# Kernel tuning notes

Measured on AMD Instinct MI355X. Metric: run time of the kernel, lower is better.

Reference implementation:

```python
import jax, jax.numpy as jnp
import numpy as np

N, E, G = 50000, 1000000, 8
H, C, L = 4, 32, 3          # heads, per-head channels, GAT layers
HID = H * C                  # 128
NODE_D, EDGE_D, REC_D = 64, 16, 8
NEG_SLOPE = 0.2              # PyG GATConv default


def setup_inputs() -> dict:
    key = jax.random.key(0)
    ks = jax.random.split(key, 24)

    def glorot(k, shape):
        fan_in = shape[-2] if len(shape) >= 2 else shape[-1]
        return jax.random.normal(k, shape, dtype=jnp.float32) / jnp.sqrt(jnp.float32(fan_in))

    inp = {
        "x": jax.random.normal(ks[0], (N, NODE_D), dtype=jnp.float32),
        "edge_index": jax.random.randint(ks[1], (2, E), 0, N, dtype=jnp.int64),
        "edge_attr": jax.random.normal(ks[2], (E, EDGE_D), dtype=jnp.float32),
        "batch": jnp.sort(jax.random.randint(ks[3], (N,), 0, G, dtype=jnp.int64)),
        "recipe": jax.random.normal(ks[4], (G, REC_D), dtype=jnp.float32),
        # input projection + edge encoder
        "W_in": glorot(ks[5], (NODE_D + REC_D, HID)),
        "b_in": jnp.zeros((HID,), jnp.float32),
        "W_edge": glorot(ks[6], (EDGE_D, HID)),
        "b_edge": jnp.zeros((HID,), jnp.float32),
        # stacked GATConv params (PyG GATConv: lin & lin_edge have no bias)
        "lin_w": glorot(ks[7], (L, HID, HID)),
        "lin_edge_w": glorot(ks[8], (L, HID, HID)),
        "att_src": glorot(ks[9], (L, H, C)),
        "att_dst": glorot(ks[10], (L, H, C)),
        "att_edge": glorot(ks[11], (L, H, C)),
        "gat_bias": jnp.zeros((L, HID), jnp.float32),
        "W1": glorot(ks[12], (HID, HID)),
        "b1": jnp.zeros((HID,), jnp.float32),
        "W2": glorot(ks[13], (HID, 1)),
        "b2": jnp.zeros((1,), jnp.float32),
    }
    return inp


def reference(x, edge_index, edge_attr, batch, recipe,
              W_in, b_in, W_edge, b_edge,
              lin_w, lin_edge_w, att_src, att_dst, att_edge, gat_bias,
              W1, b1, W2, b2):
    src, dst = edge_index[0], edge_index[1]

    # broadcast recipe to nodes, project, relu
    h = jnp.concatenate([x, recipe[batch]], axis=1)        # [N, NODE_D+REC_D]
    h = jax.nn.relu(h @ W_in + b_in)                        # [N, HID]
    e = edge_attr @ W_edge + b_edge                         # [E, HID]

    for l in range(L):
        xl = (h @ lin_w[l]).reshape(N, H, C)                # [N,H,C]
        el = (e @ lin_edge_w[l]).reshape(E, H, C)           # [E,H,C]
        a_src = jnp.sum(xl * att_src[l], axis=-1)           # [N,H]
        a_dst = jnp.sum(xl * att_dst[l], axis=-1)           # [N,H]
        a_edge = jnp.sum(el * att_edge[l], axis=-1)         # [E,H]
        alpha = jax.nn.leaky_relu(a_src[src] + a_dst[dst] + a_edge, NEG_SLOPE)
        # segment softmax over destination nodes
        amax = jax.ops.segment_max(alpha, dst, num_segments=N)   # [N,H]
        alpha = jnp.exp(alpha - amax[dst])
        denom = jax.ops.segment_sum(alpha, dst, num_segments=N)  # [N,H]
        alpha = alpha / denom[dst]
        # weighted message scatter-add (dropout is identity in eval mode)
        msg = xl[src] * alpha[..., None]                    # [E,H,C]
        out = jax.ops.segment_sum(msg, dst, num_segments=N).reshape(N, HID) + gat_bias[l]
        h = jax.nn.relu(out)

    # global mean pool over graphs
    counts = jax.ops.segment_sum(jnp.ones((N,), h.dtype), batch, num_segments=G)
    g = jax.ops.segment_sum(h, batch, num_segments=G) / jnp.maximum(counts, 1.0)[:, None]

    return jax.nn.relu(g @ W1 + b1) @ W2 + b2               # [G,1]
```

## Files before the change

kernel.cpp:

```cpp
#include <hip/hip_runtime.h>
#include <math.h>


__device__ __forceinline__ float lrelu(float x) { return x >= 0.f ? x : 0.2f * x; }

__device__ __forceinline__ unsigned pack_bf2(float a, float b) {
  unsigned ua = __float_as_uint(a), ub = __float_as_uint(b);
  ua += 0x7fffu + ((ua >> 16) & 1u);
  ub += 0x7fffu + ((ub >> 16) & 1u);
  return (ua >> 16) | (ub & 0xffff0000u);
}
__device__ __forceinline__ float bf_lo(unsigned u) { return __uint_as_float(u << 16); }
__device__ __forceinline__ float bf_hi(unsigned u) { return __uint_as_float(u & 0xffff0000u); }

__global__ void rank_kernel(const int* __restrict__ dst, int* __restrict__ deg,
                            int* __restrict__ rank, int E) {
  int e = blockIdx.x * 256 + threadIdx.x;
  if (e < E) rank[e] = atomicAdd(&deg[dst[e]], 1);
}

__global__ __launch_bounds__(1024) void scanA_kernel(const int* __restrict__ deg,
                                                     int* __restrict__ tmp,
                                                     int* __restrict__ bsum, int n) {
  __shared__ int wsum[16];
  int tid = threadIdx.x;
  int lane = tid & 63, wid = tid >> 6;
  int i = blockIdx.x * 1024 + tid;
  int v = (i < n) ? deg[i] : 0;
  int sv = v;
#pragma unroll
  for (int off = 1; off < 64; off <<= 1) {
    int t = __shfl_up(sv, off);
    if (lane >= off) sv += t;
  }
  if (lane == 63) wsum[wid] = sv;
  __syncthreads();
  if (wid == 0) {
    int wv = (lane < 16) ? wsum[lane] : 0;
#pragma unroll
    for (int off = 1; off < 16; off <<= 1) {
      int t = __shfl_up(wv, off);
      if (lane >= off) wv += t;
    }
    if (lane < 16) wsum[lane] = wv;
  }
  __syncthreads();
  int waveoff = (wid > 0) ? wsum[wid - 1] : 0;
  int incl = waveoff + sv;
  if (i < n) tmp[i] = incl;
  if (tid == 1023) bsum[blockIdx.x] = incl;
}

__global__ void scanB_kernel(int* __restrict__ bsum, int nb, int* __restrict__ total_out) {
  int lane = threadIdx.x;
  int v = (lane < nb) ? bsum[lane] : 0;
  int sv = v;
#pragma unroll
  for (int off = 1; off < 64; off <<= 1) {
    int t = __shfl_up(sv, off);
    if (lane >= off) sv += t;
  }
  if (lane < nb) bsum[lane] = sv - v;
  if (lane == 63) *total_out = sv;
}

__global__ __launch_bounds__(1024) void scanC_kernel(const int* __restrict__ deg,
                                                     const int* __restrict__ tmp,
                                                     const int* __restrict__ bsum,
                                                     int* __restrict__ row_ptr, int n) {
  int i = blockIdx.x * 1024 + threadIdx.x;
  if (i < n) row_ptr[i] = tmp[i] - deg[i] + bsum[blockIdx.x];
}

__global__ void perm_kernel(const int* __restrict__ dst, const int* __restrict__ rank,
                            const int* __restrict__ row_ptr, int* __restrict__ perm, int E) {
  int e = blockIdx.x * 256 + threadIdx.x;
  if (e < E) perm[row_ptr[dst[e]] + rank[e]] = e;
}

__global__ void prep_params(const float* __restrict__ lin_edge_w,
                            const float* __restrict__ att_edge,
                            const float* __restrict__ W_edge,
                            const float* __restrict__ b_edge,
                            float* __restrict__ Mc) {
  __shared__ float WE[128][12];
  int t = threadIdx.x;
  for (int idx = t; idx < 128 * 12; idx += 256) {
    int k = idx / 12, j = idx - k * 12;
    int l = j >> 2, h = j & 3;
    float s = 0.f;
    for (int c = 0; c < 32; ++c)
      s += lin_edge_w[((size_t)l * 128 + k) * 128 + h * 32 + c] * att_edge[(l * 4 + h) * 32 + c];
    WE[k][j] = s;
  }
  __syncthreads();
  for (int idx = t; idx < 16 * 12; idx += 256) {
    int i = idx / 12, j = idx - i * 12;
    float s = 0.f;
    for (int k = 0; k < 128; ++k) s += W_edge[i * 128 + k] * WE[k][j];
    Mc[idx] = s;
  }
  if (t < 12) {
    float s = 0.f;
    for (int k = 0; k < 128; ++k) s += b_edge[k] * WE[k][t];
    Mc[192 + t] = s;
  }
}

__global__ void edge_build_kernel(const int* __restrict__ perm,
                                  const int* __restrict__ srcA,
                                  const float* __restrict__ edge_attr,
                                  const float* __restrict__ Mc,
                                  int* __restrict__ src_csr,
                                  float* __restrict__ a_edge_csr, int E) {
  __shared__ float M[16][12];
  __shared__ float cv[12];
  int t = threadIdx.x;
  if (t < 192) M[t / 12][t % 12] = Mc[t];
  if (t < 12) cv[t] = Mc[192 + t];
  __syncthreads();
  int i = blockIdx.x * 256 + t;
  if (i >= E) return;
  int e = perm[i];
  const float4* p = (const float4*)(edge_attr + (size_t)e * 16);
  float4 v0 = p[0], v1 = p[1], v2 = p[2], v3 = p[3];
  float ea[16] = {v0.x, v0.y, v0.z, v0.w, v1.x, v1.y, v1.z, v1.w,
                  v2.x, v2.y, v2.z, v2.w, v3.x, v3.y, v3.z, v3.w};
  float a[12];
#pragma unroll
  for (int j = 0; j < 12; ++j) {
    float s = cv[j];
#pragma unroll
    for (int k = 0; k < 16; ++k) s += ea[k] * M[k][j];
    a[j] = s;
  }
  src_csr[i] = srcA[e];
#pragma unroll
  for (int l = 0; l < 3; ++l) {
    float4 o = make_float4(a[l * 4 + 0], a[l * 4 + 1], a[l * 4 + 2], a[l * 4 + 3]);
    *(float4*)(a_edge_csr + ((size_t)l * E + i) * 4) = o;
  }
}

__global__ __launch_bounds__(256) void proj_kernel(const float* __restrict__ x,
                                                   const float* __restrict__ recipe,
                                                   const int* __restrict__ batch,
                                                   const float* __restrict__ W_in,
                                                   const float* __restrict__ b_in,
                                                   float* __restrict__ h, int N) {
  __shared__ float Wc[72][128];
  __shared__ float Ac[64][72];
  int t = threadIdx.x;
  int tx = t & 31, ty = t >> 5;
  int row0 = blockIdx.x * 64;
  for (int idx = t; idx < 2304; idx += 256) {
    int k = idx >> 5, c4 = idx & 31;
    *(float4*)&Wc[k][c4 * 4] = *(const float4*)(W_in + (size_t)k * 128 + c4 * 4);
  }
  for (int idx = t; idx < 1024; idx += 256) {
    int r = idx >> 4, c4 = idx & 15;
    int row = row0 + r;
    float4 v = make_float4(0.f, 0.f, 0.f, 0.f);
    if (row < N) v = *(const float4*)(x + (size_t)row * 64 + c4 * 4);
    *(float4*)&Ac[r][c4 * 4] = v;
  }
  for (int idx = t; idx < 128; idx += 256) {
    int r = idx >> 1, c4 = idx & 1;
    int row = row0 + r;
    float4 v = make_float4(0.f, 0.f, 0.f, 0.f);
    if (row < N) v = *(const float4*)(recipe + (size_t)batch[row] * 8 + c4 * 4);
    *(float4*)&Ac[r][64 + c4 * 4] = v;
  }
  __syncthreads();
  float4 bias = *(const float4*)(b_in + tx * 4);
  float4 acc[8];
#pragma unroll
  for (int s = 0; s < 8; ++s) acc[s] = bias;
  for (int k4 = 0; k4 < 18; ++k4) {
    float4 w0 = *(float4*)&Wc[k4 * 4 + 0][tx * 4];
    float4 w1 = *(float4*)&Wc[k4 * 4 + 1][tx * 4];
    float4 w2 = *(float4*)&Wc[k4 * 4 + 2][tx * 4];
    float4 w3 = *(float4*)&Wc[k4 * 4 + 3][tx * 4];
#pragma unroll
    for (int s = 0; s < 8; ++s) {
      float4 av = *(float4*)&Ac[ty + 8 * s][k4 * 4];
      acc[s].x += av.x * w0.x + av.y * w1.x + av.z * w2.x + av.w * w3.x;
      acc[s].y += av.x * w0.y + av.y * w1.y + av.z * w2.y + av.w * w3.y;
      acc[s].z += av.x * w0.z + av.y * w1.z + av.z * w2.z + av.w * w3.z;
      acc[s].w += av.x * w0.w + av.y * w1.w + av.z * w2.w + av.w * w3.w;
    }
  }
#pragma unroll
  for (int s = 0; s < 8; ++s) {
    int row = row0 + ty + 8 * s;
    if (row < N) {
      float4 o = acc[s];
      o.x = fmaxf(o.x, 0.f); o.y = fmaxf(o.y, 0.f);
      o.z = fmaxf(o.z, 0.f); o.w = fmaxf(o.w, 0.f);
      *(float4*)(h + (size_t)row * 128 + tx * 4) = o;
    }
  }
}

__global__ __launch_bounds__(256) void gemm128_kernel(const float* __restrict__ A,
                                                      const float* __restrict__ W,
                                                      const float* __restrict__ att_s,
                                                      const float* __restrict__ att_d,
                                                      unsigned short* __restrict__ Cb,
                                                      float* __restrict__ a_src,
                                                      float* __restrict__ a_dst, int M) {
  __shared__ float Wc[32][128];
  __shared__ float Ac[64][32];
  int t = threadIdx.x;
  int tx = t & 31, ty = t >> 5;
  int row0 = blockIdx.x * 64;
  float4 acc[8];
#pragma unroll
  for (int s = 0; s < 8; ++s) acc[s] = make_float4(0.f, 0.f, 0.f, 0.f);
  for (int kc = 0; kc < 128; kc += 32) {
    for (int idx = t; idx < 1024; idx += 256) {
      int k = idx >> 5, c4 = idx & 31;
      *(float4*)&Wc[k][c4 * 4] = *(const float4*)(W + (size_t)(kc + k) * 128 + c4 * 4);
    }
    for (int idx = t; idx < 512; idx += 256) {
      int r = idx >> 3, c4 = idx & 7;
      int row = row0 + r;
      float4 v = make_float4(0.f, 0.f, 0.f, 0.f);
      if (row < M) v = *(const float4*)(A + (size_t)row * 128 + kc + c4 * 4);
      *(float4*)&Ac[r][c4 * 4] = v;
    }
    __syncthreads();
#pragma unroll
    for (int k4 = 0; k4 < 8; ++k4) {
      float4 w0 = *(float4*)&Wc[k4 * 4 + 0][tx * 4];
      float4 w1 = *(float4*)&Wc[k4 * 4 + 1][tx * 4];
      float4 w2 = *(float4*)&Wc[k4 * 4 + 2][tx * 4];
      float4 w3 = *(float4*)&Wc[k4 * 4 + 3][tx * 4];
#pragma unroll
      for (int s = 0; s < 8; ++s) {
        float4 av = *(float4*)&Ac[ty + 8 * s][k4 * 4];
        acc[s].x += av.x * w0.x + av.y * w1.x + av.z * w2.x + av.w * w3.x;
        acc[s].y += av.x * w0.y + av.y * w1.y + av.z * w2.y + av.w * w3.y;
        acc[s].z += av.x * w0.z + av.y * w1.z + av.z * w2.z + av.w * w3.z;
        acc[s].w += av.x * w0.w + av.y * w1.w + av.z * w2.w + av.w * w3.w;
      }
    }
    __syncthreads();
  }
  int hh = tx >> 3, sub = tx & 7;
  const float4 as4 = *(const float4*)(att_s + hh * 32 + sub * 4);
  const float4 ad4 = *(const float4*)(att_d + hh * 32 + sub * 4);
  float* part_s = &Wc[0][0];
  float* part_d = &Wc[16][0];
#pragma unroll
  for (int s = 0; s < 8; ++s) {
    int r = ty + 8 * s;
    int row = row0 + r;
    if (row < M) {
      uint2 pk;
      pk.x = pack_bf2(acc[s].x, acc[s].y);
      pk.y = pack_bf2(acc[s].z, acc[s].w);
      *(uint2*)(Cb + (size_t)row * 128 + tx * 4) = pk;
    }
    part_s[(r * 4 + hh) * 8 + sub] =
        acc[s].x * as4.x + acc[s].y * as4.y + acc[s].z * as4.z + acc[s].w * as4.w;
    part_d[(r * 4 + hh) * 8 + sub] =
        acc[s].x * ad4.x + acc[s].y * ad4.y + acc[s].z * ad4.z + acc[s].w * ad4.w;
  }
  __syncthreads();
  {
    int r = t >> 2, hd = t & 3;
    float ss = 0.f, dd = 0.f;
#pragma unroll
    for (int u = 0; u < 8; ++u) {
      ss += part_s[(r * 4 + hd) * 8 + u];
      dd += part_d[(r * 4 + hd) * 8 + u];
    }
    int row = row0 + r;
    if (row < M) {
      a_src[(size_t)row * 4 + hd] = ss;
      a_dst[(size_t)row * 4 + hd] = dd;
    }
  }
}

__global__ __launch_bounds__(256) void node_kernel(const int* __restrict__ row_ptr,
                                                   const int* __restrict__ src_csr,
                                                   const float* __restrict__ a_src,
                                                   const float* __restrict__ a_dst,
                                                   const float* __restrict__ aep,
                                                   const unsigned short* __restrict__ xlb,
                                                   const float* __restrict__ bias,
                                                   float* __restrict__ h_out, int N) {
  int lane = threadIdx.x & 63;
  int g = lane >> 3;
  int t = lane & 7;
  int h = t >> 1;
  int n = blockIdx.x * 4 + (threadIdx.x >> 6);
  if (n >= N) return;
  int s = row_ptr[n], e = row_ptr[n + 1];

  const float* bp = bias + t * 16;
  float* op = h_out + (size_t)n * 128 + t * 16;
  if (e <= s) {
    if (g == 0) {
#pragma unroll
      for (int q = 0; q < 4; ++q) {
        float4 b = *(const float4*)(bp + q * 4);
        float4 o = make_float4(fmaxf(b.x, 0.f), fmaxf(b.y, 0.f), fmaxf(b.z, 0.f), fmaxf(b.w, 0.f));
        *(float4*)(op + q * 4) = o;
      }
    }
    return;
  }

  float ad = a_dst[(size_t)n * 4 + h];

  float den = 0.f;
  float num[16];
#pragma unroll
  for (int c = 0; c < 16; ++c) num[c] = 0.f;

  for (int i = s + g; i < e; i += 8) {
    int sc = src_csr[i];
    float as = a_src[(size_t)sc * 4 + h];
    float ae = aep[(size_t)i * 4 + h];
    const uint4* xp = (const uint4*)(xlb + (size_t)sc * 128 + t * 16);
    uint4 u0 = xp[0], u1 = xp[1];
    float a = lrelu(as + ad + ae);
    float w = __expf(fminf(a, 80.f));
    den += w;
    num[0]  += w * bf_lo(u0.x); num[1]  += w * bf_hi(u0.x);
    num[2]  += w * bf_lo(u0.y); num[3]  += w * bf_hi(u0.y);
    num[4]  += w * bf_lo(u0.z); num[5]  += w * bf_hi(u0.z);
    num[6]  += w * bf_lo(u0.w); num[7]  += w * bf_hi(u0.w);
    num[8]  += w * bf_lo(u1.x); num[9]  += w * bf_hi(u1.x);
    num[10] += w * bf_lo(u1.y); num[11] += w * bf_hi(u1.y);
    num[12] += w * bf_lo(u1.z); num[13] += w * bf_hi(u1.z);
    num[14] += w * bf_lo(u1.w); num[15] += w * bf_hi(u1.w);
  }

#pragma unroll
  for (int off = 8; off < 64; off <<= 1) {
    den += __shfl_xor(den, off);
#pragma unroll
    for (int c = 0; c < 16; ++c) num[c] += __shfl_xor(num[c], off);
  }

  if (g == 0) {
    float rh = 1.f / den;
#pragma unroll
    for (int q = 0; q < 4; ++q) {
      float4 b = *(const float4*)(bp + q * 4);
      float4 o;
      o.x = fmaxf(num[q * 4 + 0] * rh + b.x, 0.f);
      o.y = fmaxf(num[q * 4 + 1] * rh + b.y, 0.f);
      o.z = fmaxf(num[q * 4 + 2] * rh + b.z, 0.f);
      o.w = fmaxf(num[q * 4 + 3] * rh + b.w, 0.f);
      *(float4*)(op + q * 4) = o;
    }
  }
}

__global__ void pool_kernel(const float* __restrict__ h, const int* __restrict__ batch,
                            float* __restrict__ g_sum, int* __restrict__ counts, int N) {
  int ch = threadIdx.x & 127;
  int sub = threadIdx.x >> 7;
  int per_block = (N + gridDim.x - 1) / gridDim.x;
  int start = blockIdx.x * per_block;
  int end = start + per_block;
  if (end > N) end = N;
  float acc = 0.f;
  int cnt = 0;
  int cur_g = -1;
  for (int i = start + sub; i < end; i += 2) {
    int g = batch[i];
    if (g != cur_g) {
      if (cur_g >= 0) {
        atomicAdd(&g_sum[(size_t)cur_g * 128 + ch], acc);
        if (ch == 0) atomicAdd(&counts[cur_g], cnt);
      }
      acc = 0.f;
      cnt = 0;
      cur_g = g;
    }
    acc += h[(size_t)i * 128 + ch];
    cnt += 1;
  }
  if (cur_g >= 0) {
    atomicAdd(&g_sum[(size_t)cur_g * 128 + ch], acc);
    if (ch == 0) atomicAdd(&counts[cur_g], cnt);
  }
}

__global__ void head_kernel(const float* __restrict__ g_sum, const int* __restrict__ counts,
                            const float* __restrict__ W1, const float* __restrict__ b1,
                            const float* __restrict__ W2, const float* __restrict__ b2,
                            float* __restrict__ out) {
  __shared__ float g[8][128];
  __shared__ float t1[8][128];
  int t = threadIdx.x;
  for (int idx = t; idx < 1024; idx += 256) {
    int gi = idx >> 7, ch = idx & 127;
    g[gi][ch] = g_sum[idx] / fmaxf((float)counts[gi], 1.f);
  }
  __syncthreads();
  for (int idx = t; idx < 1024; idx += 256) {
    int gi = idx >> 7, j = idx & 127;
    float a = b1[j];
    for (int k = 0; k < 128; ++k) a += g[gi][k] * W1[(size_t)k * 128 + j];
    t1[gi][j] = fmaxf(a, 0.f);
  }
  __syncthreads();
  if (t < 8) {
    float a = b2[0];
    for (int j = 0; j < 128; ++j) a += t1[t][j] * W2[j];
    out[t] = a;
  }
}

extern "C" void kernel_launch(void* const* d_in, const int* in_sizes, int n_in,
                              void* d_out, int out_size, void* d_ws, size_t ws_size,
                              hipStream_t stream) {
  const float* x         = (const float*)d_in[0];
  const int*   edge_idx  = (const int*)d_in[1];
  const float* edge_attr = (const float*)d_in[2];
  const int*   batch     = (const int*)d_in[3];
  const float* recipe    = (const float*)d_in[4];
  const float* W_in      = (const float*)d_in[5];
  const float* b_in      = (const float*)d_in[6];
  const float* W_edge    = (const float*)d_in[7];
  const float* b_edge    = (const float*)d_in[8];
  const float* lin_w     = (const float*)d_in[9];
  const float* lin_edge_w= (const float*)d_in[10];
  const float* att_src   = (const float*)d_in[11];
  const float* att_dst   = (const float*)d_in[12];
  const float* att_edge  = (const float*)d_in[13];
  const float* gat_bias  = (const float*)d_in[14];
  const float* W1        = (const float*)d_in[15];
  const float* b1        = (const float*)d_in[16];
  const float* W2        = (const float*)d_in[17];
  const float* b2p       = (const float*)d_in[18];

  const int N = in_sizes[3];
  const int E = in_sizes[1] / 2;
  const int* src = edge_idx;
  const int* dst = edge_idx + E;

  char* ws = (char*)d_ws;
  size_t off = 0;
  auto alloc = [&](size_t bytes) -> void* {
    void* p = ws + off;
    off += (bytes + 255) & ~(size_t)255;
    return p;
  };
  float* hA         = (float*)alloc((size_t)N * 128 * 4);
  float* hB         = (float*)alloc((size_t)N * 128 * 4);
  unsigned short* xlb = (unsigned short*)alloc((size_t)N * 128 * 2);
  float* a_srcA     = (float*)alloc((size_t)N * 4 * 4);
  float* a_dstA     = (float*)alloc((size_t)N * 4 * 4);
  float* a_edge_csr = (float*)alloc((size_t)3 * E * 4 * 4);
  int*   src_csr    = (int*)alloc((size_t)E * 4);
  int*   rank       = (int*)alloc((size_t)E * 4);
  int*   perm       = (int*)alloc((size_t)E * 4);
  int*   row_ptr    = (int*)alloc((size_t)(N + 1) * 4);
  int*   deg        = (int*)alloc((size_t)N * 4);
  int*   scan_tmp   = (int*)alloc((size_t)N * 4);
  int*   bsum       = (int*)alloc(64 * 4);
  float* Mc         = (float*)alloc(204 * 4);
  float* g_sum      = (float*)alloc(8 * 128 * 4);
  int*   counts     = (int*)alloc(8 * 4);
  (void)ws_size; (void)n_in; (void)out_size;

  const int eb = (E + 255) / 256;
  const int rowtiles = (N + 63) / 64;
  const int nb = (N + 1023) / 1024;

  hipMemsetAsync(deg, 0, (size_t)N * 4, stream);
  hipMemsetAsync(g_sum, 0, 8 * 128 * 4, stream);
  hipMemsetAsync(counts, 0, 8 * 4, stream);

  rank_kernel<<<eb, 256, 0, stream>>>(dst, deg, rank, E);
  scanA_kernel<<<nb, 1024, 0, stream>>>(deg, scan_tmp, bsum, N);
  scanB_kernel<<<1, 64, 0, stream>>>(bsum, nb, row_ptr + N);
  scanC_kernel<<<nb, 1024, 0, stream>>>(deg, scan_tmp, bsum, row_ptr, N);
  perm_kernel<<<eb, 256, 0, stream>>>(dst, rank, row_ptr, perm, E);
  prep_params<<<1, 256, 0, stream>>>(lin_edge_w, att_edge, W_edge, b_edge, Mc);
  edge_build_kernel<<<eb, 256, 0, stream>>>(perm, src, edge_attr, Mc,
                                            src_csr, a_edge_csr, E);
  proj_kernel<<<rowtiles, 256, 0, stream>>>(x, recipe, batch, W_in, b_in, hA, N);

  float* hcur = hA;
  float* hnxt = hB;
  for (int l = 0; l < 3; ++l) {
    gemm128_kernel<<<rowtiles, 256, 0, stream>>>(hcur, lin_w + (size_t)l * 128 * 128,
                                                 att_src + (size_t)l * 128,
                                                 att_dst + (size_t)l * 128,
                                                 xlb, a_srcA, a_dstA, N);
    node_kernel<<<(N + 3) / 4, 256, 0, stream>>>(row_ptr, src_csr, a_srcA, a_dstA,
                                                 a_edge_csr + (size_t)l * E * 4, xlb,
                                                 gat_bias + (size_t)l * 128, hnxt, N);
    float* tmp = hcur; hcur = hnxt; hnxt = tmp;
  }

  pool_kernel<<<256, 256, 0, stream>>>(hcur, batch, g_sum, counts, N);
  head_kernel<<<1, 256, 0, stream>>>(g_sum, counts, W1, b1, W2, b2p, (float*)d_out);
}
```

Baseline: 468.9 us.

## Use bf16 MFMA with split hi/lo weights for per-layer node GEMM

Replaces the fp32 FMA-based 128x128 node GEMM with a matrix-core kernel using 16x16x32 bf16 MFMA. Weights are pre-split into bf16 hi and lo parts and transposed once in a new prep kernel, while activations are rounded to bf16. The attention dot products are computed with wave shuffles instead of a shared-memory reduction. The aim is to cut GEMM compute time, at the cost of lower activation precision and uncoalesced scalar bf16 stores of the output.

```diff
diff --git a/kernel.cpp b/kernel.cpp
--- a/kernel.cpp
+++ b/kernel.cpp
@@ -1,6 +1,14 @@
 #include <hip/hip_runtime.h>
 #include <math.h>
 
+
+typedef __attribute__((ext_vector_type(8))) __bf16 bf16x8;
+typedef __attribute__((ext_vector_type(4))) float f32x4;
+
+union FragU {
+  uint4 u;
+  bf16x8 v;
+};
 
 __device__ __forceinline__ float lrelu(float x) { return x >= 0.f ? x : 0.2f * x; }
 
@@ -9,6 +17,11 @@
   ua += 0x7fffu + ((ua >> 16) & 1u);
   ub += 0x7fffu + ((ub >> 16) & 1u);
   return (ua >> 16) | (ub & 0xffff0000u);
+}
+__device__ __forceinline__ unsigned short bf_of(float a) {
+  unsigned ua = __float_as_uint(a);
+  ua += 0x7fffu + ((ua >> 16) & 1u);
+  return (unsigned short)(ua >> 16);
 }
 __device__ __forceinline__ float bf_lo(unsigned u) { return __uint_as_float(u << 16); }
 __device__ __forceinline__ float bf_hi(unsigned u) { return __uint_as_float(u & 0xffff0000u); }
@@ -107,6 +120,23 @@
   }
 }
 
+__global__ void prep_w_kernel(const float* __restrict__ lin_w,
+                              unsigned short* __restrict__ wt_hi,
+                              unsigned short* __restrict__ wt_lo) {
+  int l = blockIdx.x;
+  const float* W = lin_w + (size_t)l * 16384;
+  unsigned short* hi = wt_hi + (size_t)l * 16384;
+  unsigned short* lo = wt_lo + (size_t)l * 16384;
+  for (int idx = threadIdx.x; idx < 16384; idx += 256) {
+    int k = idx >> 7, n = idx & 127;
+    float w = W[idx];
+    unsigned short hb = bf_of(w);
+    float hf = __uint_as_float((unsigned)hb << 16);
+    hi[n * 128 + k] = hb;
+    lo[n * 128 + k] = bf_of(w - hf);
+  }
+}
+
 __global__ void edge_build_kernel(const int* __restrict__ perm,
                                   const int* __restrict__ srcA,
                                   const float* __restrict__ edge_attr,
@@ -202,84 +232,78 @@
   }
 }
 
-__global__ __launch_bounds__(256) void gemm128_kernel(const float* __restrict__ A,
-                                                      const float* __restrict__ W,
-                                                      const float* __restrict__ att_s,
-                                                      const float* __restrict__ att_d,
-                                                      unsigned short* __restrict__ Cb,
-                                                      float* __restrict__ a_src,
-                                                      float* __restrict__ a_dst, int M) {
-  __shared__ float Wc[32][128];
-  __shared__ float Ac[64][32];
+__global__ __launch_bounds__(256) void gemm_mfma_kernel(
+    const float* __restrict__ A, const unsigned short* __restrict__ wt_hi,
+    const unsigned short* __restrict__ wt_lo,
+    const float* __restrict__ att_s, const float* __restrict__ att_d,
+    unsigned short* __restrict__ Cb, float* __restrict__ a_src,
+    float* __restrict__ a_dst, int M) {
   int t = threadIdx.x;
-  int tx = t & 31, ty = t >> 5;
-  int row0 = blockIdx.x * 64;
-  float4 acc[8];
-#pragma unroll
-  for (int s = 0; s < 8; ++s) acc[s] = make_float4(0.f, 0.f, 0.f, 0.f);
-  for (int kc = 0; kc < 128; kc += 32) {
-    for (int idx = t; idx < 1024; idx += 256) {
-      int k = idx >> 5, c4 = idx & 31;
-      *(float4*)&Wc[k][c4 * 4] = *(const float4*)(W + (size_t)(kc + k) * 128 + c4 * 4);
-    }
-    for (int idx = t; idx < 512; idx += 256) {
-      int r = idx >> 3, c4 = idx & 7;
-      int row = row0 + r;
-      float4 v = make_float4(0.f, 0.f, 0.f, 0.f);
-      if (row < M) v = *(const float4*)(A + (size_t)row * 128 + kc + c4 * 4);
-      *(float4*)&Ac[r][c4 * 4] = v;
-    }
-    __syncthreads();
-#pragma unroll
-    for (int k4 = 0; k4 < 8; ++k4) {
-      float4 w0 = *(float4*)&Wc[k4 * 4 + 0][tx * 4];
-      float4 w1 = *(float4*)&Wc[k4 * 4 + 1][tx * 4];
-      float4 w2 = *(float4*)&Wc[k4 * 4 + 2][tx * 4];
-      float4 w3 = *(float4*)&Wc[k4 * 4 + 3][tx * 4];
-#pragma unroll
-      for (int s = 0; s < 8; ++s) {
-        float4 av = *(float4*)&Ac[ty + 8 * s][k4 * 4];
-        acc[s].x += av.x * w0.x + av.y * w1.x + av.z * w2.x + av.w * w3.x;
-        acc[s].y += av.x * w0.y + av.y * w1.y + av.z * w2.y + av.w * w3.y;
-        acc[s].z += av.x * w0.z + av.y * w1.z + av.z * w2.z + av.w * w3.z;
-        acc[s].w += av.x * w0.w + av.y * w1.w + av.z * w2.w + av.w * w3.w;
+  int lane = t & 63, w = t >> 6;
+  int c = lane & 15, q = lane >> 4;
+  int m0 = blockIdx.x * 64 + w * 16;
+  int rowA = m0 + c;
+  bool rowok = rowA < M;
+
+  f32x4 acc[8];
+#pragma unroll
+  for (int n = 0; n < 8; ++n) acc[n] = 0.f;
+
+#pragma unroll
+  for (int kk = 0; kk < 128; kk += 32) {
+    float4 fa0 = make_float4(0.f, 0.f, 0.f, 0.f), fa1 = fa0;
+    if (rowok) {
+      const float* ap = A + (size_t)rowA * 128 + kk + 8 * q;
+      fa0 = *(const float4*)ap;
+      fa1 = *(const float4*)(ap + 4);
+    }
+    FragU af;
+    af.u.x = pack_bf2(fa0.x, fa0.y);
+    af.u.y = pack_bf2(fa0.z, fa0.w);
+    af.u.z = pack_bf2(fa1.x, fa1.y);
+    af.u.w = pack_bf2(fa1.z, fa1.w);
+    const unsigned short* bhp = wt_hi + (size_t)c * 128 + kk + 8 * q;
+    const unsigned short* blp = wt_lo + (size_t)c * 128 + kk + 8 * q;
+#pragma unroll
+    for (int n = 0; n < 8; ++n) {
+      FragU bh, bl;
+      bh.u = *(const uint4*)(bhp + n * 2048);
+      bl.u = *(const uint4*)(blp + n * 2048);
+      acc[n] = __builtin_amdgcn_mfma_f32_16x16x32_bf16(af.v, bh.v, acc[n], 0, 0, 0);
+      acc[n] = __builtin_amdgcn_mfma_f32_16x16x32_bf16(af.v, bl.v, acc[n], 0, 0, 0);
+    }
+  }
+
+  float asr[4][2], adr[4][2];
+#pragma unroll
+  for (int hh = 0; hh < 4; ++hh) {
+    asr[hh][0] = att_s[32 * hh + c];
+    asr[hh][1] = att_s[32 * hh + 16 + c];
+    adr[hh][0] = att_d[32 * hh + c];
+    adr[hh][1] = att_d[32 * hh + 16 + c];
+  }
+#pragma unroll
+  for (int i = 0; i < 4; ++i) {
+    int row = m0 + 4 * q + i;
+    bool ok = row < M;
+    if (ok) {
+      size_t base = (size_t)row * 128;
+#pragma unroll
+      for (int n = 0; n < 8; ++n) Cb[base + n * 16 + c] = bf_of(acc[n][i]);
+    }
+#pragma unroll
+    for (int hh = 0; hh < 4; ++hh) {
+      float ps = acc[2 * hh][i] * asr[hh][0] + acc[2 * hh + 1][i] * asr[hh][1];
+      float pd = acc[2 * hh][i] * adr[hh][0] + acc[2 * hh + 1][i] * adr[hh][1];
+#pragma unroll
+      for (int off = 1; off < 16; off <<= 1) {
+        ps += __shfl_xor(ps, off);
+        pd += __shfl_xor(pd, off);
       }
-    }
-    __syncthreads();
-  }
-  int hh = tx >> 3, sub = tx & 7;
-  const float4 as4 = *(const float4*)(att_s + hh * 32 + sub * 4);
-  const float4 ad4 = *(const float4*)(att_d + hh * 32 + sub * 4);
-  float* part_s = &Wc[0][0];
-  float* part_d = &Wc[16][0];
-#pragma unroll
-  for (int s = 0; s < 8; ++s) {
-    int r = ty + 8 * s;
-    int row = row0 + r;
-    if (row < M) {
-      uint2 pk;
-      pk.x = pack_bf2(acc[s].x, acc[s].y);
-      pk.y = pack_bf2(acc[s].z, acc[s].w);
-      *(uint2*)(Cb + (size_t)row * 128 + tx * 4) = pk;
-    }
-    part_s[(r * 4 + hh) * 8 + sub] =
-        acc[s].x * as4.x + acc[s].y * as4.y + acc[s].z * as4.z + acc[s].w * as4.w;
-    part_d[(r * 4 + hh) * 8 + sub] =
-        acc[s].x * ad4.x + acc[s].y * ad4.y + acc[s].z * ad4.z + acc[s].w * ad4.w;
-  }
-  __syncthreads();
-  {
-    int r = t >> 2, hd = t & 3;
-    float ss = 0.f, dd = 0.f;
-#pragma unroll
-    for (int u = 0; u < 8; ++u) {
-      ss += part_s[(r * 4 + hd) * 8 + u];
-      dd += part_d[(r * 4 + hd) * 8 + u];
-    }
-    int row = row0 + r;
-    if (row < M) {
-      a_src[(size_t)row * 4 + hd] = ss;
-      a_dst[(size_t)row * 4 + hd] = dd;
+      if (ok && c == hh) {
+        a_src[(size_t)row * 4 + hh] = ps;
+        a_dst[(size_t)row * 4 + hh] = pd;
+      }
     }
   }
 }
@@ -468,6 +492,8 @@
   int*   scan_tmp   = (int*)alloc((size_t)N * 4);
   int*   bsum       = (int*)alloc(64 * 4);
   float* Mc         = (float*)alloc(204 * 4);
+  unsigned short* wt_hi = (unsigned short*)alloc((size_t)3 * 16384 * 2);
+  unsigned short* wt_lo = (unsigned short*)alloc((size_t)3 * 16384 * 2);
   float* g_sum      = (float*)alloc(8 * 128 * 4);
   int*   counts     = (int*)alloc(8 * 4);
   (void)ws_size; (void)n_in; (void)out_size;
@@ -486,6 +512,7 @@
   scanC_kernel<<<nb, 1024, 0, stream>>>(deg, scan_tmp, bsum, row_ptr, N);
   perm_kernel<<<eb, 256, 0, stream>>>(dst, rank, row_ptr, perm, E);
   prep_params<<<1, 256, 0, stream>>>(lin_edge_w, att_edge, W_edge, b_edge, Mc);
+  prep_w_kernel<<<3, 256, 0, stream>>>(lin_w, wt_hi, wt_lo);
   edge_build_kernel<<<eb, 256, 0, stream>>>(perm, src, edge_attr, Mc,
                                             src_csr, a_edge_csr, E);
   proj_kernel<<<rowtiles, 256, 0, stream>>>(x, recipe, batch, W_in, b_in, hA, N);
@@ -493,10 +520,12 @@
   float* hcur = hA;
   float* hnxt = hB;
   for (int l = 0; l < 3; ++l) {
-    gemm128_kernel<<<rowtiles, 256, 0, stream>>>(hcur, lin_w + (size_t)l * 128 * 128,
-                                                 att_src + (size_t)l * 128,
-                                                 att_dst + (size_t)l * 128,
-                                                 xlb, a_srcA, a_dstA, N);
+    gemm_mfma_kernel<<<rowtiles, 256, 0, stream>>>(hcur,
+                                                   wt_hi + (size_t)l * 16384,
+                                                   wt_lo + (size_t)l * 16384,
+                                                   att_src + (size_t)l * 128,
+                                                   att_dst + (size_t)l * 128,
+                                                   xlb, a_srcA, a_dstA, N);
     node_kernel<<<(N + 3) / 4, 256, 0, stream>>>(row_ptr, src_csr, a_srcA, a_dstA,
                                                  a_edge_csr + (size_t)l * E * 4, xlb,
                                                  gat_bias + (size_t)l * 128, hnxt, N);
```

Result: slower. 491.5 us (median of 5 runs) (+4.8%).
